# Optimization experiments

Measured on AMD Instinct MI355X. Metric: run time of the kernel, lower is better.

The kernel has to match this reference:

```python
import jax, jax.numpy as jnp
import numpy as np

EPS = 1e-10
TEMP = 1.0
N_ITERS = 21  # 20 + int(1.0 / temp)


def _sinkhorn(log_alpha, temp, n_iters):
    # log_alpha: (..., n, n). Alternating row/col log-normalization in log space.
    la = log_alpha / temp
    for _ in range(n_iters):
        la = la - jax.scipy.special.logsumexp(la, axis=-2, keepdims=True)
        la = la - jax.scipy.special.logsumexp(la, axis=-1, keepdims=True)
    return jnp.exp(la)


def setup_inputs() -> dict:
    key = jax.random.key(0)
    k1, k2, k3 = jax.random.split(key, 3)
    B, N, S = 256, 1024, 16
    x = jax.random.normal(k1, (B, N), dtype=jnp.float32)
    log_alpha = jax.random.normal(k2, (N, N), dtype=jnp.float32)  # learned param (init was gumbel noise)
    u = jax.random.uniform(k3, (S, N, N), dtype=jnp.float32)  # uniform draws for Gumbel noise
    return {"x": x, "log_alpha": log_alpha, "u": u}


def reference(x, log_alpha, u):
    # Gumbel noise from uniform draws: -log(eps - log(U + eps))
    noise = -jnp.log(EPS - jnp.log(u + EPS))  # (S, N, N)
    log_alpha_noise = log_alpha[None, :, :] + noise
    soft_perms = _sinkhorn(log_alpha_noise, TEMP, N_ITERS)  # (S, N, N)
    # x: (B, N) -> (1, B, N) @ (S, N, N) -> (S, B, N)
    return jnp.einsum('bn,snm->sbm', x, soft_perms)
```

## Files before the change

### kernel.cpp

```cpp
#include <hip/hip_runtime.h>
#include <math.h>

static constexpr int S_ = 16;
static constexpr int N_ = 1024;
static constexpr int B_ = 256;
static constexpr int ITERS = 21;
#define EPSC 1e-10f

using short8 = __attribute__((ext_vector_type(8))) short;
using f32x4  = __attribute__((ext_vector_type(4))) float;

__device__ __forceinline__ float bf2f(unsigned short h) {
    union { unsigned int u; float f; } v; v.u = ((unsigned int)h) << 16; return v.f;
}
__device__ __forceinline__ unsigned short f2bf(float f) {
    union { float f; unsigned int u; } v; v.f = f;
    unsigned int r = v.u + 0x7fffu + ((v.u >> 16) & 1u);
    return (unsigned short)(r >> 16);
}
__device__ __forceinline__ unsigned int pack2(float a, float b) {
    return (unsigned int)f2bf(a) | ((unsigned int)f2bf(b) << 16);
}

__device__ __forceinline__ float la0_of(float uv, float lav) {
    float t1 = __logf(uv + EPSC);
    float t2 = EPSC - t1;
    return lav - __logf(t2);
}

#define MAP_S_SLAB(bid, s, slab) \
    const int s = ((bid) & 7) + 8 * (((bid) >> 3) & 1); \
    const int slab = (bid) >> 4;

__global__ void __launch_bounds__(256)
build_K2(const float* __restrict__ u, const float* __restrict__ la,
         unsigned short* __restrict__ Kb, float* __restrict__ partial) {
    MAP_S_SLAB(blockIdx.x, s, slab)
    const int t = threadIdx.x, wv = t >> 6, l = t & 63;
    float cs[16];
    #pragma unroll
    for (int e = 0; e < 16; ++e) cs[e] = 0.f;

    const int i0 = slab * 16 + wv * 4;
    #pragma unroll
    for (int rr = 0; rr < 4; ++rr) {
        const int i = i0 + rr;
        const float* up  = u  + ((size_t)s * N_ + i) * N_;
        const float* lap = la + (size_t)i * N_;
        float kf[16];
        #pragma unroll
        for (int h = 0; h < 2; ++h) {
            const int c = h * 512 + 8 * l;
            float4 ua = *(const float4*)(up + c);
            float4 ub = *(const float4*)(up + c + 4);
            float4 la4 = *(const float4*)(lap + c);
            float4 lb4 = *(const float4*)(lap + c + 4);
            const float uf[8] = {ua.x, ua.y, ua.z, ua.w, ub.x, ub.y, ub.z, ub.w};
            const float lf[8] = {la4.x, la4.y, la4.z, la4.w, lb4.x, lb4.y, lb4.z, lb4.w};
            unsigned int pk[4];
            #pragma unroll
            for (int e = 0; e < 4; ++e) {
                float k0 = __expf(lf[2*e])   / (EPSC - __logf(uf[2*e]   + EPSC));
                float k1 = __expf(lf[2*e+1]) / (EPSC - __logf(uf[2*e+1] + EPSC));
                unsigned short b0 = f2bf(k0), b1 = f2bf(k1);
                pk[e] = (unsigned int)b0 | ((unsigned int)b1 << 16);
                kf[h*8 + 2*e]     = bf2f(b0);
                kf[h*8 + 2*e + 1] = bf2f(b1);
            }
            *(uint4*)(Kb + ((size_t)s * N_ + i) * N_ + c) =
                make_uint4(pk[0], pk[1], pk[2], pk[3]);
        }
        #pragma unroll
        for (int e = 0; e < 16; ++e) cs[e] += kf[e];
    }

    __shared__ float lds[4][1024];
    *(float4*)&lds[wv][8*l]       = make_float4(cs[0], cs[1], cs[2], cs[3]);
    *(float4*)&lds[wv][8*l + 4]   = make_float4(cs[4], cs[5], cs[6], cs[7]);
    *(float4*)&lds[wv][512 + 8*l]     = make_float4(cs[8], cs[9], cs[10], cs[11]);
    *(float4*)&lds[wv][512 + 8*l + 4] = make_float4(cs[12], cs[13], cs[14], cs[15]);
    __syncthreads();
    const int j = t * 4;
    float4 p0 = *(const float4*)&lds[0][j];
    float4 p1 = *(const float4*)&lds[1][j];
    float4 p2 = *(const float4*)&lds[2][j];
    float4 p3 = *(const float4*)&lds[3][j];
    float4 o;
    o.x = p0.x + p1.x + p2.x + p3.x;  o.y = p0.y + p1.y + p2.y + p3.y;
    o.z = p0.z + p1.z + p2.z + p3.z;  o.w = p0.w + p1.w + p2.w + p3.w;
    *(float4*)(partial + ((size_t)s * 64 + slab) * N_ + j) = o;
}

__global__ void __launch_bounds__(256)
reduce_V(const float* __restrict__ partial, float* __restrict__ V) {
    const int s = blockIdx.x >> 2;
    const int j = (blockIdx.x & 3) * 256 + threadIdx.x;
    const float* p = partial + (size_t)s * 64 * N_ + j;
    float acc = 0.f;
    #pragma unroll
    for (int q = 0; q < 64; ++q) acc += p[(size_t)q * N_];
    V[s * N_ + j] = 1.0f / acc;
}

__global__ void __launch_bounds__(256)
sink_iter(const unsigned short* __restrict__ Kb, const float* __restrict__ V,
          float* __restrict__ U, float* __restrict__ partial) {
    MAP_S_SLAB(blockIdx.x, s, slab)
    const int t = threadIdx.x, wv = t >> 6, l = t & 63;

    float v[16];
    const float* Vp = V + s * N_;
    *(float4*)&v[0]  = *(const float4*)(Vp + 8*l);
    *(float4*)&v[4]  = *(const float4*)(Vp + 8*l + 4);
    *(float4*)&v[8]  = *(const float4*)(Vp + 512 + 8*l);
    *(float4*)&v[12] = *(const float4*)(Vp + 512 + 8*l + 4);

    float cs[16];
    #pragma unroll
    for (int e = 0; e < 16; ++e) cs[e] = 0.f;

    const int i0 = slab * 16 + wv * 4;
    const unsigned short* rowp = Kb + ((size_t)s * N_ + i0) * N_;
    #pragma unroll
    for (int rr = 0; rr < 4; ++rr, rowp += N_) {
        uint4 ka = *(const uint4*)(rowp + 8*l);
        uint4 kb = *(const uint4*)(rowp + 512 + 8*l);
        float kf[16];
        kf[0]  = bf2f((unsigned short)(ka.x & 0xffffu)); kf[1]  = bf2f((unsigned short)(ka.x >> 16));
        kf[2]  = bf2f((unsigned short)(ka.y & 0xffffu)); kf[3]  = bf2f((unsigned short)(ka.y >> 16));
        kf[4]  = bf2f((unsigned short)(ka.z & 0xffffu)); kf[5]  = bf2f((unsigned short)(ka.z >> 16));
        kf[6]  = bf2f((unsigned short)(ka.w & 0xffffu)); kf[7]  = bf2f((unsigned short)(ka.w >> 16));
        kf[8]  = bf2f((unsigned short)(kb.x & 0xffffu)); kf[9]  = bf2f((unsigned short)(kb.x >> 16));
        kf[10] = bf2f((unsigned short)(kb.y & 0xffffu)); kf[11] = bf2f((unsigned short)(kb.y >> 16));
        kf[12] = bf2f((unsigned short)(kb.z & 0xffffu)); kf[13] = bf2f((unsigned short)(kb.z >> 16));
        kf[14] = bf2f((unsigned short)(kb.w & 0xffffu)); kf[15] = bf2f((unsigned short)(kb.w >> 16));
        float dot = 0.f;
        #pragma unroll
        for (int e = 0; e < 16; ++e) dot += kf[e] * v[e];
        #pragma unroll
        for (int m = 32; m >= 1; m >>= 1) dot += __shfl_xor(dot, m);
        const float ui = 1.0f / dot;
        if (l == 0) U[s * N_ + i0 + rr] = ui;
        #pragma unroll
        for (int e = 0; e < 16; ++e) cs[e] += kf[e] * ui;
    }

    __shared__ float lds[4][1024];
    *(float4*)&lds[wv][8*l]       = make_float4(cs[0], cs[1], cs[2], cs[3]);
    *(float4*)&lds[wv][8*l + 4]   = make_float4(cs[4], cs[5], cs[6], cs[7]);
    *(float4*)&lds[wv][512 + 8*l]     = make_float4(cs[8], cs[9], cs[10], cs[11]);
    *(float4*)&lds[wv][512 + 8*l + 4] = make_float4(cs[12], cs[13], cs[14], cs[15]);
    __syncthreads();
    const int j = t * 4;
    float4 p0 = *(const float4*)&lds[0][j];
    float4 p1 = *(const float4*)&lds[1][j];
    float4 p2 = *(const float4*)&lds[2][j];
    float4 p3 = *(const float4*)&lds[3][j];
    float4 o;
    o.x = p0.x + p1.x + p2.x + p3.x;  o.y = p0.y + p1.y + p2.y + p3.y;
    o.z = p0.z + p1.z + p2.z + p3.z;  o.w = p0.w + p1.w + p2.w + p3.w;
    *(float4*)(partial + ((size_t)s * 64 + slab) * N_ + j) = o;
}

__global__ void __launch_bounds__(256)
transpose_K(const unsigned short* __restrict__ Kb, unsigned short* __restrict__ KbT) {
    const int s = blockIdx.z, k0 = blockIdx.x * 64, m0 = blockIdx.y * 64;
    __shared__ unsigned short tile[64][66];
    const int t = threadIdx.x, c4 = (t & 15) * 4, rr = t >> 4;
    const unsigned short* src = Kb + (size_t)s * N_ * N_;
    unsigned short* dst = KbT + (size_t)s * N_ * N_;
    #pragma unroll
    for (int q = 0; q < 4; ++q) {
        const int r = q * 16 + rr;
        ushort4 v = *(const ushort4*)(src + (size_t)(k0 + r) * N_ + m0 + c4);
        tile[r][c4] = v.x; tile[r][c4 + 1] = v.y; tile[r][c4 + 2] = v.z; tile[r][c4 + 3] = v.w;
    }
    __syncthreads();
    #pragma unroll
    for (int q = 0; q < 4; ++q) {
        const int rm = q * 16 + rr;
        ushort4 v;
        v.x = tile[c4][rm]; v.y = tile[c4 + 1][rm];
        v.z = tile[c4 + 2][rm]; v.w = tile[c4 + 3][rm];
        *(ushort4*)(dst + (size_t)(m0 + rm) * N_ + k0 + c4) = v;
    }
}

__global__ void __launch_bounds__(256)
mfma_out(const float* __restrict__ x, const unsigned short* __restrict__ KbT,
         const float* __restrict__ U, const float* __restrict__ V,
         float* __restrict__ out) {
    const int s  = blockIdx.z;
    const int m0 = blockIdx.x * 64;
    const int b0 = blockIdx.y * 128;
    const int t  = threadIdx.x;
    const int wid = t >> 6, l = t & 63;
    const int wr = wid >> 1, wc = wid & 1;

    __shared__ alignas(16) unsigned short lsA[128 * 64];
    __shared__ alignas(16) unsigned short lsB[64 * 64];

    f32x4 acc[4][2];
    #pragma unroll
    for (int fi = 0; fi < 4; ++fi)
        #pragma unroll
        for (int fj = 0; fj < 2; ++fj)
            acc[fi][fj] = (f32x4){0.f, 0.f, 0.f, 0.f};

    const unsigned short* Bp = KbT + ((size_t)s * N_ + m0) * N_;
    const float* Up = U + s * N_;

    float4 xa[4], xb[4];
    uint4  kv[2];
    float4 ua[2], ub[2];

    auto load_tile = [&](int k0) {
        #pragma unroll
        for (int i = 0; i < 4; ++i) {
            const int Lb  = i * 4096 + t * 16;
            const int row = Lb >> 7;
            const int kb  = Lb & 127;
            const float* xp = x + (size_t)(b0 + row) * N_ + k0 + (kb >> 1);
            xa[i] = *(const float4*)xp;
            xb[i] = *(const float4*)(xp + 4);
        }
        #pragma unroll
        for (int i = 0; i < 2; ++i) {
            const int Lb  = i * 4096 + t * 16;
            const int row = Lb >> 7;
            const int kb  = Lb & 127;
            kv[i] = *(const uint4*)((const char*)Bp + (size_t)row * 2048 + (k0 << 1) + kb);
            const int ke = k0 + (kb >> 1);
            ua[i] = *(const float4*)(Up + ke);
            ub[i] = *(const float4*)(Up + ke + 4);
        }
    };

    load_tile(0);
    for (int k0 = 0; k0 < N_; k0 += 64) {
        __syncthreads();
        #pragma unroll
        for (int i = 0; i < 4; ++i) {
            const int Lb  = i * 4096 + t * 16;
            const int row = Lb >> 7;
            const int kb  = Lb & 127;
            uint4 pk = make_uint4(pack2(xa[i].x, xa[i].y), pack2(xa[i].z, xa[i].w),
                                  pack2(xb[i].x, xb[i].y), pack2(xb[i].z, xb[i].w));
            *(uint4*)((char*)lsA + (row << 7) + (kb ^ ((row & 7) << 4))) = pk;
        }
        #pragma unroll
        for (int i = 0; i < 2; ++i) {
            const int Lb  = i * 4096 + t * 16;
            const int row = Lb >> 7;
            const int kb  = Lb & 127;
            uint4 pk;
            pk.x = pack2(bf2f((unsigned short)(kv[i].x & 0xffffu)) * ua[i].x,
                         bf2f((unsigned short)(kv[i].x >> 16))     * ua[i].y);
            pk.y = pack2(bf2f((unsigned short)(kv[i].y & 0xffffu)) * ua[i].z,
                         bf2f((unsigned short)(kv[i].y >> 16))     * ua[i].w);
            pk.z = pack2(bf2f((unsigned short)(kv[i].z & 0xffffu)) * ub[i].x,
                         bf2f((unsigned short)(kv[i].z >> 16))     * ub[i].y);
            pk.w = pack2(bf2f((unsigned short)(kv[i].w & 0xffffu)) * ub[i].z,
                         bf2f((unsigned short)(kv[i].w >> 16))     * ub[i].w);
            *(uint4*)((char*)lsB + (row << 7) + (kb ^ ((row & 7) << 4))) = pk;
        }
        __syncthreads();
        if (k0 + 64 < N_) load_tile(k0 + 64);
        #pragma unroll
        for (int ks = 0; ks < 2; ++ks) {
            const int koff = ks * 64 + ((l >> 4) << 4);
            short8 afr[4], bfr[2];
            #pragma unroll
            for (int fi = 0; fi < 4; ++fi) {
                const int r = wr * 64 + fi * 16 + (l & 15);
                afr[fi] = *(const short8*)((const char*)lsA + (r << 7) + (koff ^ ((r & 7) << 4)));
            }
            #pragma unroll
            for (int fj = 0; fj < 2; ++fj) {
                const int r = wc * 32 + fj * 16 + (l & 15);
                bfr[fj] = *(const short8*)((const char*)lsB + (r << 7) + (koff ^ ((r & 7) << 4)));
            }
            #pragma unroll
            for (int fi = 0; fi < 4; ++fi)
                #pragma unroll
                for (int fj = 0; fj < 2; ++fj)
                    acc[fi][fj] = __builtin_amdgcn_mfma_f32_16x16x32_bf16(
                        afr[fi], bfr[fj], acc[fi][fj], 0, 0, 0);
        }
    }
    #pragma unroll
    for (int fj = 0; fj < 2; ++fj) {
        const int m = m0 + wc * 32 + fj * 16 + (l & 15);
        const float vm = V[s * N_ + m];
        #pragma unroll
        for (int fi = 0; fi < 4; ++fi) {
            const int b = b0 + wr * 64 + fi * 16 + ((l >> 4) << 2);
            float* op = out + ((size_t)s * B_ + b) * N_ + m;
            #pragma unroll
            for (int e = 0; e < 4; ++e)
                op[(size_t)e * N_] = acc[fi][fj][e] * vm;
        }
    }
}

__global__ void __launch_bounds__(256)
transpose_x(const float* __restrict__ x, float* __restrict__ xT) {
    __shared__ float tile[32][33];
    const int tx = threadIdx.x, ty = threadIdx.y;
    const int gx = blockIdx.x * 32, gy = blockIdx.y * 32;
    #pragma unroll
    for (int i = 0; i < 4; ++i)
        tile[ty + i * 8][tx] = x[(gy + ty + i * 8) * N_ + gx + tx];
    __syncthreads();
    #pragma unroll
    for (int i = 0; i < 4; ++i)
        xT[(size_t)(gx + ty + i * 8) * B_ + gy + tx] = tile[tx][ty + i * 8];
}

__global__ void __launch_bounds__(256)
col_pass(const float* __restrict__ u, const float* __restrict__ la,
         const float* __restrict__ r, float* __restrict__ c) {
    const int s = blockIdx.y, t = threadIdx.x;
    const int tx = t & 15, rg = t >> 4;
    const int j = blockIdx.x * 16 + tx;
    __shared__ alignas(16) float r_lds[N_];
    ((float4*)r_lds)[t] = ((const float4*)(r + s * N_))[t];
    __syncthreads();
    const float cj = c[s * N_ + j];
    const float* up = u + (size_t)s * N_ * N_;
    const int i0 = rg * 64;
    float acc = 0.f;
    #pragma unroll 4
    for (int ii = 0; ii < 64; ++ii) {
        const int i = i0 + ii;
        acc += __expf(la0_of(up[(size_t)i * N_ + j], la[i * N_ + j]) - r_lds[i] - cj);
    }
    __shared__ float sums[16][17];
    sums[rg][tx] = acc;
    __syncthreads();
    if (t < 16) {
        float tot = 0.f;
        #pragma unroll
        for (int k = 0; k < 16; ++k) tot += sums[k][t];
        c[s * N_ + blockIdx.x * 16 + t] = cj + __logf(tot);
    }
}

__global__ void __launch_bounds__(256)
row_pass(const float* __restrict__ u, const float* __restrict__ la,
         const float* __restrict__ c, float* __restrict__ r) {
    const int s = blockIdx.y, t = threadIdx.x;
    const int w = t >> 6, l = t & 63;
    const int i = blockIdx.x * 4 + w;
    __shared__ alignas(16) float c_lds[N_];
    ((float4*)c_lds)[t] = ((const float4*)(c + s * N_))[t];
    __syncthreads();
    const float ri = r[s * N_ + i];
    const float* up = u + (size_t)s * N_ * N_ + (size_t)i * N_;
    const float* lap = la + (size_t)i * N_;
    float acc = 0.f;
    #pragma unroll
    for (int k = 0; k < 16; ++k) {
        const int jj = l + (k << 6);
        acc += __expf(la0_of(up[jj], lap[jj]) - c_lds[jj] - ri);
    }
    #pragma unroll
    for (int m = 32; m >= 1; m >>= 1) acc += __shfl_xor(acc, m);
    if (l == 0) r[s * N_ + i] = ri + __logf(acc);
}

__global__ void __launch_bounds__(256)
matmul_out(const float* __restrict__ u, const float* __restrict__ la,
           const float* __restrict__ xT, const float* __restrict__ r,
           const float* __restrict__ c, float* __restrict__ out) {
    const int s = blockIdx.z, m0 = blockIdx.x * 64, b0 = blockIdx.y * 128;
    const int t = threadIdx.x, tx = t & 7, ty = t >> 3;
    __shared__ alignas(16) float Bs[16][64];
    float acc[4][8] = {};
    const float* up = u + (size_t)s * N_ * N_;
    const float* rp = r + s * N_;
    for (int k0 = 0; k0 < N_; k0 += 16) {
        __syncthreads();
        {
            const int kk = t >> 4, f4 = t & 15;
            const int k = k0 + kk;
            const float rk = rp[k];
            const float4 uv = *(const float4*)(up + (size_t)k * N_ + m0 + f4 * 4);
            const float4 lv = *(const float4*)(la + (size_t)k * N_ + m0 + f4 * 4);
            float4 p;
            p.x = __expf(la0_of(uv.x, lv.x) - rk);
            p.y = __expf(la0_of(uv.y, lv.y) - rk);
            p.z = __expf(la0_of(uv.z, lv.z) - rk);
            p.w = __expf(la0_of(uv.w, lv.w) - rk);
            *(float4*)(&Bs[kk][f4 * 4]) = p;
        }
        __syncthreads();
        #pragma unroll
        for (int kk = 0; kk < 16; ++kk) {
            const float4 a4 = *(const float4*)(xT + (size_t)(k0 + kk) * B_ + b0 + ty * 4);
            const float4 bA = *(const float4*)(&Bs[kk][tx * 8]);
            const float4 bB = *(const float4*)(&Bs[kk][tx * 8 + 4]);
            const float av[4] = {a4.x, a4.y, a4.z, a4.w};
            const float bv[8] = {bA.x, bA.y, bA.z, bA.w, bB.x, bB.y, bB.z, bB.w};
            #pragma unroll
            for (int rr = 0; rr < 4; ++rr)
                #pragma unroll
                for (int cc = 0; cc < 8; ++cc)
                    acc[rr][cc] += av[rr] * bv[cc];
        }
    }
    float cm[8];
    #pragma unroll
    for (int cc = 0; cc < 8; ++cc) cm[cc] = __expf(-c[s * N_ + m0 + tx * 8 + cc]);
    #pragma unroll
    for (int rr = 0; rr < 4; ++rr) {
        float4 o0, o1;
        o0.x = acc[rr][0] * cm[0]; o0.y = acc[rr][1] * cm[1];
        o0.z = acc[rr][2] * cm[2]; o0.w = acc[rr][3] * cm[3];
        o1.x = acc[rr][4] * cm[4]; o1.y = acc[rr][5] * cm[5];
        o1.z = acc[rr][6] * cm[6]; o1.w = acc[rr][7] * cm[7];
        float* op = out + ((size_t)s * B_ + b0 + ty * 4 + rr) * N_ + m0 + tx * 8;
        *(float4*)op       = o0;
        *(float4*)(op + 4) = o1;
    }
}

extern "C" void kernel_launch(void* const* d_in, const int* in_sizes, int n_in,
                              void* d_out, int out_size, void* d_ws, size_t ws_size,
                              hipStream_t stream) {
    (void)in_sizes; (void)n_in; (void)out_size;
    const float* x  = (const float*)d_in[0];
    const float* la = (const float*)d_in[1];
    const float* u  = (const float*)d_in[2];
    float* out = (float*)d_out;

    const size_t KN = (size_t)S_ * N_ * N_;
    const size_t need = KN * 2 * 2
                      + (size_t)2 * S_ * N_ * 4;

    if (ws_size >= need) {
        unsigned short* Kb  = (unsigned short*)d_ws;
        unsigned short* KbT = Kb + KN;
        float* partial = (float*)KbT;
        float* U = (float*)(KbT + KN);
        float* V = U + S_ * N_;

        build_K2<<<1024, 256, 0, stream>>>(u, la, Kb, partial);

        for (int it = 0; it < ITERS; ++it) {
            reduce_V<<<64, 256, 0, stream>>>(partial, V);
            sink_iter<<<1024, 256, 0, stream>>>(Kb, V, U, partial);
        }

        transpose_K<<<dim3(16, 16, 16), 256, 0, stream>>>(Kb, KbT);

        mfma_out<<<dim3(N_ / 64, B_ / 128, S_), 256, 0, stream>>>(x, KbT, U, V, out);
    } else {
        float* r  = (float*)d_ws;
        float* c  = r + S_ * N_;
        float* xT = c + S_ * N_;
        hipMemsetAsync(d_ws, 0, 2 * S_ * N_ * sizeof(float), stream);
        transpose_x<<<dim3(N_ / 32, B_ / 32), dim3(32, 8), 0, stream>>>(x, xT);
        for (int it = 0; it < ITERS; ++it) {
            col_pass<<<dim3(N_ / 16, S_), 256, 0, stream>>>(u, la, r, c);
            row_pass<<<dim3(N_ / 4, S_),  256, 0, stream>>>(u, la, c, r);
        }
        matmul_out<<<dim3(N_ / 64, B_ / 128, S_), 256, 0, stream>>>(u, la, xT, r, c, out);
    }
}
```

Baseline: 272.2 us.

## Fuse Sinkhorn build and iterations into one persistent kernel with per-sample barriers

Replaces the build kernel and the 21 pairs of reduce_V/sink_iter launches with a single persistent kernel of 512 blocks. Each block owns 32 rows of one sample, and blocks synchronise through per-sample atomic-counter barriers in global memory. The column-sum reduction is spread across the blocks, each reducing 32 columns. This removes about 43 kernel launches and their gaps. It relies on all 512 blocks being resident at once (launch_bounds 256,2), and the barrier has a spin timeout that could silently break correctness if the blocks are not co-resident.

```diff
diff --git a/kernel.cpp b/kernel.cpp
--- a/kernel.cpp
+++ b/kernel.cpp
@@ -28,138 +28,187 @@
     return lav - __logf(t2);
 }
 
-#define MAP_S_SLAB(bid, s, slab) \
-    const int s = ((bid) & 7) + 8 * (((bid) >> 3) & 1); \
-    const int slab = (bid) >> 4;
-
-__global__ void __launch_bounds__(256)
-build_K2(const float* __restrict__ u, const float* __restrict__ la,
-         unsigned short* __restrict__ Kb, float* __restrict__ partial) {
-    MAP_S_SLAB(blockIdx.x, s, slab)
+__device__ __forceinline__ void unpack16(const uint4& a, const uint4& b, float* kf) {
+    kf[0]  = bf2f((unsigned short)(a.x & 0xffffu)); kf[1]  = bf2f((unsigned short)(a.x >> 16));
+    kf[2]  = bf2f((unsigned short)(a.y & 0xffffu)); kf[3]  = bf2f((unsigned short)(a.y >> 16));
+    kf[4]  = bf2f((unsigned short)(a.z & 0xffffu)); kf[5]  = bf2f((unsigned short)(a.z >> 16));
+    kf[6]  = bf2f((unsigned short)(a.w & 0xffffu)); kf[7]  = bf2f((unsigned short)(a.w >> 16));
+    kf[8]  = bf2f((unsigned short)(b.x & 0xffffu)); kf[9]  = bf2f((unsigned short)(b.x >> 16));
+    kf[10] = bf2f((unsigned short)(b.y & 0xffffu)); kf[11] = bf2f((unsigned short)(b.y >> 16));
+    kf[12] = bf2f((unsigned short)(b.z & 0xffffu)); kf[13] = bf2f((unsigned short)(b.z >> 16));
+    kf[14] = bf2f((unsigned short)(b.w & 0xffffu)); kf[15] = bf2f((unsigned short)(b.w >> 16));
+}
+
+#define VIDX(c) ((c) + ((c) >> 3))
+
+__device__ __forceinline__ void sample_barrier(unsigned int* c, unsigned int expected) {
+    __syncthreads();
+    if (threadIdx.x == 0) {
+        __hip_atomic_fetch_add(c, 1u, __ATOMIC_RELEASE, __HIP_MEMORY_SCOPE_AGENT);
+        unsigned int spins = 0;
+        while (__hip_atomic_load(c, __ATOMIC_RELAXED, __HIP_MEMORY_SCOPE_AGENT) < expected) {
+            __builtin_amdgcn_s_sleep(8);
+            if (++spins > (1u << 22)) break;
+        }
+    }
+    __syncthreads();
+    asm volatile("" ::: "memory");
+}
+
+__global__ void __launch_bounds__(256, 2)
+sinkhorn_persist(const float* __restrict__ u, const float* __restrict__ la,
+                 unsigned short* __restrict__ Kb, float* __restrict__ partial,
+                 float* __restrict__ Uv, float* __restrict__ Vv,
+                 unsigned int* __restrict__ cnt) {
+    const int bid  = blockIdx.x;
+    const int s    = (bid & 7) + 8 * ((bid >> 3) & 1);
+    const int slab = bid >> 4;
     const int t = threadIdx.x, wv = t >> 6, l = t & 63;
+    const int r0 = slab * 32 + wv * 8;
+
+    __shared__ float comb[4][1024];
+    __shared__ float ldsv[1152];
+
+    unsigned int* cb = cnt + s * 64;
+    float* pbase = partial + (size_t)s * 32 * 1024;
+
     float cs[16];
     #pragma unroll
     for (int e = 0; e < 16; ++e) cs[e] = 0.f;
 
-    const int i0 = slab * 16 + wv * 4;
-    #pragma unroll
-    for (int rr = 0; rr < 4; ++rr) {
-        const int i = i0 + rr;
-        const float* up  = u  + ((size_t)s * N_ + i) * N_;
-        const float* lap = la + (size_t)i * N_;
-        float kf[16];
-        #pragma unroll
-        for (int h = 0; h < 2; ++h) {
-            const int c = h * 512 + 8 * l;
-            float4 ua = *(const float4*)(up + c);
-            float4 ub = *(const float4*)(up + c + 4);
-            float4 la4 = *(const float4*)(lap + c);
-            float4 lb4 = *(const float4*)(lap + c + 4);
-            const float uf[8] = {ua.x, ua.y, ua.z, ua.w, ub.x, ub.y, ub.z, ub.w};
-            const float lf[8] = {la4.x, la4.y, la4.z, la4.w, lb4.x, lb4.y, lb4.z, lb4.w};
-            unsigned int pk[4];
-            #pragma unroll
-            for (int e = 0; e < 4; ++e) {
-                float k0 = __expf(lf[2*e])   / (EPSC - __logf(uf[2*e]   + EPSC));
-                float k1 = __expf(lf[2*e+1]) / (EPSC - __logf(uf[2*e+1] + EPSC));
-                unsigned short b0 = f2bf(k0), b1 = f2bf(k1);
-                pk[e] = (unsigned int)b0 | ((unsigned int)b1 << 16);
-                kf[h*8 + 2*e]     = bf2f(b0);
-                kf[h*8 + 2*e + 1] = bf2f(b1);
+    #pragma unroll 1
+    for (int g = 0; g < 4; ++g) {
+        f32x4 uu[2][4];
+        float4 ll[2][4];
+        #pragma unroll
+        for (int rr = 0; rr < 2; ++rr) {
+            const int i = r0 + g * 2 + rr;
+            const float* up  = u  + ((size_t)s * N_ + i) * N_ + 8 * l;
+            const float* lap = la + (size_t)i * N_ + 8 * l;
+            uu[rr][0] = __builtin_nontemporal_load((const f32x4*)(up));
+            uu[rr][1] = __builtin_nontemporal_load((const f32x4*)(up + 4));
+            uu[rr][2] = __builtin_nontemporal_load((const f32x4*)(up + 512));
+            uu[rr][3] = __builtin_nontemporal_load((const f32x4*)(up + 516));
+            ll[rr][0] = *(const float4*)(lap);
+            ll[rr][1] = *(const float4*)(lap + 4);
+            ll[rr][2] = *(const float4*)(lap + 512);
+            ll[rr][3] = *(const float4*)(lap + 516);
+        }
+        #pragma unroll
+        for (int rr = 0; rr < 2; ++rr) {
+            const int i = r0 + g * 2 + rr;
+            #pragma unroll
+            for (int h = 0; h < 2; ++h) {
+                const float uf[8] = {uu[rr][2*h][0], uu[rr][2*h][1], uu[rr][2*h][2], uu[rr][2*h][3],
+                                     uu[rr][2*h+1][0], uu[rr][2*h+1][1], uu[rr][2*h+1][2], uu[rr][2*h+1][3]};
+                const float lf[8] = {ll[rr][2*h].x, ll[rr][2*h].y, ll[rr][2*h].z, ll[rr][2*h].w,
+                                     ll[rr][2*h+1].x, ll[rr][2*h+1].y, ll[rr][2*h+1].z, ll[rr][2*h+1].w};
+                unsigned int pk[4];
+                #pragma unroll
+                for (int e = 0; e < 4; ++e) {
+                    float k0 = __expf(lf[2*e])   / (EPSC - __logf(uf[2*e]   + EPSC));
+                    float k1 = __expf(lf[2*e+1]) / (EPSC - __logf(uf[2*e+1] + EPSC));
+                    unsigned short b0 = f2bf(k0), b1 = f2bf(k1);
+                    pk[e] = (unsigned int)b0 | ((unsigned int)b1 << 16);
+                    cs[h*8 + 2*e]     += bf2f(b0);
+                    cs[h*8 + 2*e + 1] += bf2f(b1);
+                }
+                *(uint4*)(Kb + ((size_t)s * N_ + i) * N_ + h * 512 + 8 * l) =
+                    make_uint4(pk[0], pk[1], pk[2], pk[3]);
             }
-            *(uint4*)(Kb + ((size_t)s * N_ + i) * N_ + c) =
-                make_uint4(pk[0], pk[1], pk[2], pk[3]);
-        }
-        #pragma unroll
-        for (int e = 0; e < 16; ++e) cs[e] += kf[e];
-    }
-
-    __shared__ float lds[4][1024];
-    *(float4*)&lds[wv][8*l]       = make_float4(cs[0], cs[1], cs[2], cs[3]);
-    *(float4*)&lds[wv][8*l + 4]   = make_float4(cs[4], cs[5], cs[6], cs[7]);
-    *(float4*)&lds[wv][512 + 8*l]     = make_float4(cs[8], cs[9], cs[10], cs[11]);
-    *(float4*)&lds[wv][512 + 8*l + 4] = make_float4(cs[12], cs[13], cs[14], cs[15]);
-    __syncthreads();
-    const int j = t * 4;
-    float4 p0 = *(const float4*)&lds[0][j];
-    float4 p1 = *(const float4*)&lds[1][j];
-    float4 p2 = *(const float4*)&lds[2][j];
-    float4 p3 = *(const float4*)&lds[3][j];
-    float4 o;
-    o.x = p0.x + p1.x + p2.x + p3.x;  o.y = p0.y + p1.y + p2.y + p3.y;
-    o.z = p0.z + p1.z + p2.z + p3.z;  o.w = p0.w + p1.w + p2.w + p3.w;
-    *(float4*)(partial + ((size_t)s * 64 + slab) * N_ + j) = o;
-}
-
-__global__ void __launch_bounds__(256)
-reduce_V(const float* __restrict__ partial, float* __restrict__ V) {
-    const int s = blockIdx.x >> 2;
-    const int j = (blockIdx.x & 3) * 256 + threadIdx.x;
-    const float* p = partial + (size_t)s * 64 * N_ + j;
-    float acc = 0.f;
-    #pragma unroll
-    for (int q = 0; q < 64; ++q) acc += p[(size_t)q * N_];
-    V[s * N_ + j] = 1.0f / acc;
-}
-
-__global__ void __launch_bounds__(256)
-sink_iter(const unsigned short* __restrict__ Kb, const float* __restrict__ V,
-          float* __restrict__ U, float* __restrict__ partial) {
-    MAP_S_SLAB(blockIdx.x, s, slab)
-    const int t = threadIdx.x, wv = t >> 6, l = t & 63;
-
-    float v[16];
-    const float* Vp = V + s * N_;
-    *(float4*)&v[0]  = *(const float4*)(Vp + 8*l);
-    *(float4*)&v[4]  = *(const float4*)(Vp + 8*l + 4);
-    *(float4*)&v[8]  = *(const float4*)(Vp + 512 + 8*l);
-    *(float4*)&v[12] = *(const float4*)(Vp + 512 + 8*l + 4);
-
-    float cs[16];
-    #pragma unroll
-    for (int e = 0; e < 16; ++e) cs[e] = 0.f;
-
-    const int i0 = slab * 16 + wv * 4;
-    const unsigned short* rowp = Kb + ((size_t)s * N_ + i0) * N_;
-    #pragma unroll
-    for (int rr = 0; rr < 4; ++rr, rowp += N_) {
-        uint4 ka = *(const uint4*)(rowp + 8*l);
-        uint4 kb = *(const uint4*)(rowp + 512 + 8*l);
-        float kf[16];
-        kf[0]  = bf2f((unsigned short)(ka.x & 0xffffu)); kf[1]  = bf2f((unsigned short)(ka.x >> 16));
-        kf[2]  = bf2f((unsigned short)(ka.y & 0xffffu)); kf[3]  = bf2f((unsigned short)(ka.y >> 16));
-        kf[4]  = bf2f((unsigned short)(ka.z & 0xffffu)); kf[5]  = bf2f((unsigned short)(ka.z >> 16));
-        kf[6]  = bf2f((unsigned short)(ka.w & 0xffffu)); kf[7]  = bf2f((unsigned short)(ka.w >> 16));
-        kf[8]  = bf2f((unsigned short)(kb.x & 0xffffu)); kf[9]  = bf2f((unsigned short)(kb.x >> 16));
-        kf[10] = bf2f((unsigned short)(kb.y & 0xffffu)); kf[11] = bf2f((unsigned short)(kb.y >> 16));
-        kf[12] = bf2f((unsigned short)(kb.z & 0xffffu)); kf[13] = bf2f((unsigned short)(kb.z >> 16));
-        kf[14] = bf2f((unsigned short)(kb.w & 0xffffu)); kf[15] = bf2f((unsigned short)(kb.w >> 16));
-        float dot = 0.f;
-        #pragma unroll
-        for (int e = 0; e < 16; ++e) dot += kf[e] * v[e];
-        #pragma unroll
-        for (int m = 32; m >= 1; m >>= 1) dot += __shfl_xor(dot, m);
-        const float ui = 1.0f / dot;
-        if (l == 0) U[s * N_ + i0 + rr] = ui;
-        #pragma unroll
-        for (int e = 0; e < 16; ++e) cs[e] += kf[e] * ui;
-    }
-
-    __shared__ float lds[4][1024];
-    *(float4*)&lds[wv][8*l]       = make_float4(cs[0], cs[1], cs[2], cs[3]);
-    *(float4*)&lds[wv][8*l + 4]   = make_float4(cs[4], cs[5], cs[6], cs[7]);
-    *(float4*)&lds[wv][512 + 8*l]     = make_float4(cs[8], cs[9], cs[10], cs[11]);
-    *(float4*)&lds[wv][512 + 8*l + 4] = make_float4(cs[12], cs[13], cs[14], cs[15]);
-    __syncthreads();
-    const int j = t * 4;
-    float4 p0 = *(const float4*)&lds[0][j];
-    float4 p1 = *(const float4*)&lds[1][j];
-    float4 p2 = *(const float4*)&lds[2][j];
-    float4 p3 = *(const float4*)&lds[3][j];
-    float4 o;
-    o.x = p0.x + p1.x + p2.x + p3.x;  o.y = p0.y + p1.y + p2.y + p3.y;
-    o.z = p0.z + p1.z + p2.z + p3.z;  o.w = p0.w + p1.w + p2.w + p3.w;
-    *(float4*)(partial + ((size_t)s * 64 + slab) * N_ + j) = o;
+        }
+    }
+
+    auto combine_store = [&]() {
+        __syncthreads();
+        *(float4*)&comb[wv][8*l]           = make_float4(cs[0], cs[1], cs[2], cs[3]);
+        *(float4*)&comb[wv][8*l + 4]       = make_float4(cs[4], cs[5], cs[6], cs[7]);
+        *(float4*)&comb[wv][512 + 8*l]     = make_float4(cs[8], cs[9], cs[10], cs[11]);
+        *(float4*)&comb[wv][512 + 8*l + 4] = make_float4(cs[12], cs[13], cs[14], cs[15]);
+        __syncthreads();
+        #pragma unroll
+        for (int e = 0; e < 4; ++e) {
+            const int col = t + 256 * e;
+            float x = comb[0][col] + comb[1][col] + comb[2][col] + comb[3][col];
+            __hip_atomic_store(pbase + (size_t)slab * 1024 + col, x,
+                               __ATOMIC_RELAXED, __HIP_MEMORY_SCOPE_AGENT);
+        }
+    };
+    auto vreduce = [&]() {
+        if (t < 32) {
+            const int col = slab * 32 + t;
+            float acc = 0.f;
+            #pragma unroll
+            for (int q = 0; q < 32; ++q)
+                acc += __hip_atomic_load(pbase + (size_t)q * 1024 + col,
+                                         __ATOMIC_RELAXED, __HIP_MEMORY_SCOPE_AGENT);
+            __hip_atomic_store(Vv + s * N_ + col, 1.0f / acc,
+                               __ATOMIC_RELAXED, __HIP_MEMORY_SCOPE_AGENT);
+        }
+    };
+
+    combine_store();
+    sample_barrier(cb + 0, 32);
+    vreduce();
+    sample_barrier(cb + 1, 32);
+
+    const unsigned short* rowbase = Kb + ((size_t)s * N_ + r0) * N_ + 8 * l;
+
+    #pragma unroll 1
+    for (int it = 1; it <= ITERS; ++it) {
+        {
+            float* Vp = Vv + s * N_;
+            float a0 = __hip_atomic_load(Vp + t,       __ATOMIC_RELAXED, __HIP_MEMORY_SCOPE_AGENT);
+            float a1 = __hip_atomic_load(Vp + 256 + t, __ATOMIC_RELAXED, __HIP_MEMORY_SCOPE_AGENT);
+            float a2 = __hip_atomic_load(Vp + 512 + t, __ATOMIC_RELAXED, __HIP_MEMORY_SCOPE_AGENT);
+            float a3 = __hip_atomic_load(Vp + 768 + t, __ATOMIC_RELAXED, __HIP_MEMORY_SCOPE_AGENT);
+            __syncthreads();
+            ldsv[VIDX(t)]       = a0;
+            ldsv[VIDX(256 + t)] = a1;
+            ldsv[VIDX(512 + t)] = a2;
+            ldsv[VIDX(768 + t)] = a3;
+            __syncthreads();
+        }
+        float v[16];
+        #pragma unroll
+        for (int e = 0; e < 8; ++e) {
+            v[e]     = ldsv[VIDX(8 * l + e)];
+            v[8 + e] = ldsv[VIDX(512 + 8 * l + e)];
+        }
+        #pragma unroll
+        for (int e = 0; e < 16; ++e) cs[e] = 0.f;
+
+        #pragma unroll
+        for (int g = 0; g < 2; ++g) {
+            uint4 ra[4], rb[4];
+            #pragma unroll
+            for (int rr = 0; rr < 4; ++rr) {
+                const size_t off = (size_t)(g * 4 + rr) * N_;
+                ra[rr] = *(const uint4*)(rowbase + off);
+                rb[rr] = *(const uint4*)(rowbase + off + 512);
+            }
+            #pragma unroll
+            for (int rr = 0; rr < 4; ++rr) {
+                float kf[16];
+                unpack16(ra[rr], rb[rr], kf);
+                float dot = 0.f;
+                #pragma unroll
+                for (int e = 0; e < 16; ++e) dot += kf[e] * v[e];
+                #pragma unroll
+                for (int m = 32; m >= 1; m >>= 1) dot += __shfl_xor(dot, m);
+                const float ui = 1.0f / dot;
+                if (l == 0) Uv[s * N_ + r0 + g * 4 + rr] = ui;
+                #pragma unroll
+                for (int e = 0; e < 16; ++e) cs[e] += kf[e] * ui;
+            }
+        }
+
+        if (it == ITERS) break;
+        combine_store();
+        sample_barrier(cb + 2 * it, 32);
+        vreduce();
+        sample_barrier(cb + 2 * it + 1, 32);
+    }
 }
 
 __global__ void __launch_bounds__(256)
@@ -435,8 +484,10 @@
     float* out = (float*)d_out;
 
     const size_t KN = (size_t)S_ * N_ * N_;
+    const size_t CNT_BYTES = 16 * 64 * sizeof(unsigned int);
     const size_t need = KN * 2 * 2
-                      + (size_t)2 * S_ * N_ * 4;
+                      + (size_t)2 * S_ * N_ * 4
+                      + CNT_BYTES;
 
     if (ws_size >= need) {
         unsigned short* Kb  = (unsigned short*)d_ws;
@@ -444,13 +495,11 @@
         float* partial = (float*)KbT;
         float* U = (float*)(KbT + KN);
         float* V = U + S_ * N_;
-
-        build_K2<<<1024, 256, 0, stream>>>(u, la, Kb, partial);
-
-        for (int it = 0; it < ITERS; ++it) {
-            reduce_V<<<64, 256, 0, stream>>>(partial, V);
-            sink_iter<<<1024, 256, 0, stream>>>(Kb, V, U, partial);
-        }
+        unsigned int* cnt = (unsigned int*)(V + S_ * N_);
+
+        (void)hipMemsetAsync(cnt, 0, CNT_BYTES, stream);
+
+        sinkhorn_persist<<<512, 256, 0, stream>>>(u, la, Kb, partial, U, V, cnt);
 
         transpose_K<<<dim3(16, 16, 16), 256, 0, stream>>>(Kb, KbT);
 
@@ -459,7 +508,7 @@
         float* r  = (float*)d_ws;
         float* c  = r + S_ * N_;
         float* xT = c + S_ * N_;
-        hipMemsetAsync(d_ws, 0, 2 * S_ * N_ * sizeof(float), stream);
+        (void)hipMemsetAsync(d_ws, 0, 2 * S_ * N_ * sizeof(float), stream);
         transpose_x<<<dim3(N_ / 32, B_ / 32), dim3(32, 8), 0, stream>>>(x, xT);
         for (int it = 0; it < ITERS; ++it) {
             col_pass<<<dim3(N_ / 16, S_), 256, 0, stream>>>(u, la, r, c);
```

Measured after the change: 641.4 us. +135.6%, slower.
